# Performance work log

Measured on AMD Instinct MI355X. Metric: run time of the kernel, lower is better.

## Reference

```python
import math
import jax, jax.numpy as jnp
import numpy as np

LMAX = 2


def _cg_complex(j1, m1, j2, m2, j3, m3):
    # Standard (Racah) Clebsch-Gordan coefficient <j1 m1 j2 m2 | j3 m3> for integer l.
    if m1 + m2 != m3 or j3 < abs(j1 - j2) or j3 > j1 + j2:
        return 0.0
    f = math.factorial
    pre = math.sqrt((2 * j3 + 1) * f(j3 + j1 - j2) * f(j3 - j1 + j2) * f(j1 + j2 - j3) / f(j1 + j2 + j3 + 1))
    pre *= math.sqrt(f(j3 + m3) * f(j3 - m3) * f(j1 - m1) * f(j1 + m1) * f(j2 - m2) * f(j2 + m2))
    kmin = max(0, j2 - j3 - m1, j1 + m2 - j3)
    kmax = min(j1 + j2 - j3, j1 - m1, j2 + m2)
    s = 0.0
    for k in range(kmin, kmax + 1):
        s += (-1.0) ** k / (f(k) * f(j1 + j2 - j3 - k) * f(j1 - m1 - k) * f(j2 + m2 - k) * f(j3 - j2 + m1 + k) * f(j3 - j1 - m2 + k))
    return pre * s


def _u_matrix(l):
    # Unitary map from complex SH (Condon-Shortley) to real SH, rows = real mu, cols = complex m.
    U = np.zeros((2 * l + 1, 2 * l + 1), dtype=np.complex128)
    U[l, l] = 1.0
    isq2 = 1.0 / math.sqrt(2.0)
    for m in range(1, l + 1):
        U[l + m, l - m] = isq2
        U[l + m, l + m] = ((-1.0) ** m) * isq2
        U[l - m, l - m] = 1j * isq2
        U[l - m, l + m] = -1j * ((-1.0) ** m) * isq2
    return U


def _real_clebsch_gordan(lmax):
    # Dense real-SH CG tensor over combined s=(l,m) indices, shape [S,S,S], S=(lmax+1)^2.
    S = (lmax + 1) ** 2
    cg = np.zeros((S, S, S))
    for l1 in range(lmax + 1):
        for l2 in range(lmax + 1):
            for l3 in range(abs(l1 - l2), min(lmax, l1 + l2) + 1):
                blk = np.zeros((2 * l1 + 1, 2 * l2 + 1, 2 * l3 + 1))
                for i1, m1 in enumerate(range(-l1, l1 + 1)):
                    for i2, m2 in enumerate(range(-l2, l2 + 1)):
                        for i3, m3 in enumerate(range(-l3, l3 + 1)):
                            blk[i1, i2, i3] = _cg_complex(l1, m1, l2, m2, l3, m3)
                U1, U2, U3 = _u_matrix(l1), _u_matrix(l2), _u_matrix(l3)
                r = np.einsum('am,bn,co,mno->abc', U1, U2, U3.conj(), blk.astype(np.complex128))
                r = r.real if (l1 + l2 + l3) % 2 == 0 else r.imag  # parity-dependent real part
                cg[l1 * l1:(l1 + 1) ** 2, l2 * l2:(l2 + 1) ** 2, l3 * l3:(l3 + 1) ** 2] = r
    return cg


def _sparse_cg(lmax):
    cg = _real_clebsch_gordan(lmax)
    i1, i2, i3 = np.nonzero(np.abs(cg) > 1e-10)
    vals = cg[i1, i2, i3].astype(np.float32)
    widx = np.floor(np.sqrt(i3.astype(np.float64))).astype(np.int32)  # l of output combined index
    return vals, i1.astype(np.int32), i2.astype(np.int32), i3.astype(np.int32), widx


def _spherical_harmonics_l2(d):
    # Real SH up to l=2, 'component' normalization (|x|=1 assumed). Order: (l,m) = (0,0),(1,-1),(1,0),(1,1),(2,-2..2).
    x, y, z = d[..., 0], d[..., 1], d[..., 2]
    s3, s5, s15 = math.sqrt(3.0), math.sqrt(5.0), math.sqrt(15.0)
    return jnp.stack([
        jnp.ones_like(x),
        s3 * y, s3 * z, s3 * x,
        s15 * x * y, s15 * y * z, 0.5 * s5 * (3.0 * z * z - 1.0), s15 * x * z, 0.5 * s15 * (x * x - y * y),
    ], axis=-1)


def setup_inputs():
    N_ATOMS, N_EDGES, N_BASIS, N_RADIAL = 1200, 12000, 128, 20
    S = (LMAX + 1) ** 2
    key = jax.random.key(0)
    ks = jax.random.split(key, 8)
    vals, i1, i2, i3, widx = _sparse_cg(LMAX)
    return {
        'x': jax.random.normal(ks[0], (N_ATOMS, S, N_BASIS), jnp.float32),
        'radial_ij': jax.random.uniform(ks[1], (N_EDGES, N_RADIAL), jnp.float32),
        'dir_ij': jax.random.normal(ks[2], (N_EDGES, 3), jnp.float32),
        'cutoff_ij': jax.random.uniform(ks[3], (N_EDGES, 1), jnp.float32),
        'W_filter': jax.random.normal(ks[6], (N_RADIAL, N_BASIS * (LMAX + 1)), jnp.float32) / math.sqrt(N_RADIAL),
        'b_filter': jnp.zeros((N_BASIS * (LMAX + 1),), jnp.float32),
        'cg_vals': jnp.asarray(vals),
        'idx_i': jax.random.randint(ks[4], (N_EDGES,), 0, N_ATOMS),
        'idx_j': jax.random.randint(ks[5], (N_EDGES,), 0, N_ATOMS),
        'cg_idx_in1': jnp.asarray(i1),
        'cg_idx_in2': jnp.asarray(i2),
        'cg_idx_out': jnp.asarray(i3),
        'w_idx': jnp.asarray(widx),
    }


def reference(x, radial_ij, dir_ij, cutoff_ij, W_filter, b_filter, cg_vals,
              idx_i, idx_j, cg_idx_in1, cg_idx_in2, cg_idx_out, w_idx):
    n_atoms, S, F = x.shape
    E = dir_ij.shape[0]
    d = dir_ij / jnp.linalg.norm(dir_ij, axis=-1, keepdims=True)
    Y = _spherical_harmonics_l2(d)                        # [E, S]
    Wij = (radial_ij @ W_filter + b_filter) * cutoff_ij   # [E, (lmax+1)*F]
    Wij = Wij.reshape(E, LMAX + 1, F)                     # per-l radial filter
    xj = x[idx_j]                                         # [E, S, F] neighbor features
    # Sparse CG tensor-product contraction over combined (l,m) indices.
    v = (Y[:, cg_idx_in2, None] * cg_vals[None, :, None]
         * Wij[:, w_idx, :] * xj[:, cg_idx_in1, :])       # [E, n_cg, F]
    yij = jnp.zeros((E, S, F), v.dtype).at[:, cg_idx_out, :].add(v)
    return jax.ops.segment_sum(yij, idx_i, num_segments=n_atoms)
```

## Files before the change

### kernel.cpp

```cpp
#include <hip/hip_runtime.h>
#include <math.h>


#define S9    9
#define NF    128
#define NRAD  20
#define CHUNK 16

__global__ void hist_kernel(const int* __restrict__ idx_i, int E, int* __restrict__ counts) {
    int e = blockIdx.x * blockDim.x + threadIdx.x;
    if (e < E) atomicAdd(&counts[idx_i[e]], 1);
}

__global__ __launch_bounds__(256) void scan_kernel(const int* __restrict__ counts, int A,
                                                   int* __restrict__ offsets, int* __restrict__ cursor) {
    __shared__ int part[256];
    const int t = threadIdx.x;
    const int base = t * 8;
    int c[8];
    int s = 0;
    #pragma unroll
    for (int p = 0; p < 8; ++p) {
        int idx = base + p;
        c[p] = (idx < A) ? counts[idx] : 0;
        s += c[p];
    }
    part[t] = s;
    __syncthreads();
    #pragma unroll
    for (int off = 1; off < 256; off <<= 1) {
        int v = (t >= off) ? part[t - off] : 0;
        __syncthreads();
        part[t] += v;
        __syncthreads();
    }
    int run = part[t] - s;
    #pragma unroll
    for (int p = 0; p < 8; ++p) {
        int idx = base + p;
        if (idx < A) { offsets[idx] = run; cursor[idx] = run; run += c[p]; }
    }
    if (t == 255) offsets[A] = run;
}

__global__ void scatter_kernel(const int* __restrict__ idx_i, int E,
                               int* __restrict__ cursor, int* __restrict__ esorted) {
    int e = blockIdx.x * blockDim.x + threadIdx.x;
    if (e < E) {
        int p = atomicAdd(&cursor[idx_i[e]], 1);
        esorted[p] = e;
    }
}

__global__ __launch_bounds__(128) void so3_atom_kernel(
    const float* __restrict__ x,
    const float* __restrict__ radial,
    const float* __restrict__ dir,
    const float* __restrict__ cutoff,
    const float* __restrict__ Wf,
    const float* __restrict__ bf,
    const float* __restrict__ cg_vals,
    const int* __restrict__ idx_j,
    const int* __restrict__ cg_i1,
    const int* __restrict__ cg_i2,
    const int* __restrict__ cg_i3,
    int ncg,
    const int* __restrict__ offsets,
    const int* __restrict__ esorted,
    float* __restrict__ out)
{
    const int a = blockIdx.x;
    const int f = threadIdx.x;
    const int start = offsets[a];
    const int end   = offsets[a + 1];

    __shared__ float M[CHUNK][81];
    __shared__ float Ysh[CHUNK][9];
    __shared__ int   els[CHUNK];

    float acc[S9];
    #pragma unroll
    for (int s = 0; s < S9; ++s) acc[s] = 0.0f;

    const float b0 = bf[0 * NF + f];
    const float b1 = bf[1 * NF + f];
    const float b2 = bf[2 * NF + f];

    for (int cs = start; cs < end; cs += CHUNK) {
        const int n = min(CHUNK, end - cs);

        for (int q = f; q < n * 81; q += NF) ((float*)M)[q] = 0.0f;

        if (f < n) {
            const int e = esorted[cs + f];
            els[f] = e;
            float dx = dir[3 * e], dy = dir[3 * e + 1], dz = dir[3 * e + 2];
            const float inv = rsqrtf(dx * dx + dy * dy + dz * dz);
            dx *= inv; dy *= inv; dz *= inv;
            const float s3c  = 1.7320508075688772f;
            const float s5c  = 2.2360679774997896f;
            const float s15c = 3.8729833462074170f;
            Ysh[f][0] = 1.0f;
            Ysh[f][1] = s3c * dy;
            Ysh[f][2] = s3c * dz;
            Ysh[f][3] = s3c * dx;
            Ysh[f][4] = s15c * dx * dy;
            Ysh[f][5] = s15c * dy * dz;
            Ysh[f][6] = 0.5f * s5c * (3.0f * dz * dz - 1.0f);
            Ysh[f][7] = s15c * dx * dz;
            Ysh[f][8] = 0.5f * s15c * (dx * dx - dy * dy);
        }
        __syncthreads();

        for (int c = 0; c < n; ++c) {
            for (int k = f; k < ncg; k += NF) {
                atomicAdd(&M[c][cg_i3[k] * S9 + cg_i1[k]], cg_vals[k] * Ysh[c][cg_i2[k]]);
            }
        }
        __syncthreads();

        for (int c = 0; c < n; ++c) {
            const int e = els[c];

            float rad[NRAD];
            #pragma unroll
            for (int r = 0; r < NRAD; ++r) rad[r] = radial[e * NRAD + r];
            const float cut = cutoff[e];

            float wl0 = b0, wl1 = b1, wl2 = b2;
            #pragma unroll
            for (int r = 0; r < NRAD; ++r) {
                const float* wrow = Wf + r * (3 * NF) + f;
                wl0 = fmaf(rad[r], wrow[0],      wl0);
                wl1 = fmaf(rad[r], wrow[NF],     wl1);
                wl2 = fmaf(rad[r], wrow[2 * NF], wl2);
            }
            wl0 *= cut; wl1 *= cut; wl2 *= cut;

            const int j = idx_j[e];
            const float* xp = x + (size_t)j * (S9 * NF) + f;
            float xj[S9];
            #pragma unroll
            for (int s = 0; s < S9; ++s) xj[s] = xp[s * NF];

            const float* Mc = M[c];
            #pragma unroll
            for (int s3 = 0; s3 < S9; ++s3) {
                float t = 0.0f;
                #pragma unroll
                for (int s1 = 0; s1 < S9; ++s1) t = fmaf(Mc[s3 * S9 + s1], xj[s1], t);
                const float w = (s3 == 0) ? wl0 : ((s3 < 4) ? wl1 : wl2);
                acc[s3] = fmaf(w, t, acc[s3]);
            }
        }
        __syncthreads();
    }

    float* op = out + (size_t)a * (S9 * NF) + f;
    #pragma unroll
    for (int s = 0; s < S9; ++s) op[s * NF] = acc[s];
}

extern "C" void kernel_launch(void* const* d_in, const int* in_sizes, int n_in,
                              void* d_out, int out_size, void* d_ws, size_t ws_size,
                              hipStream_t stream) {
    const float* x       = (const float*)d_in[0];
    const float* radial  = (const float*)d_in[1];
    const float* dir     = (const float*)d_in[2];
    const float* cutoff  = (const float*)d_in[3];
    const float* Wf      = (const float*)d_in[4];
    const float* bf      = (const float*)d_in[5];
    const float* cg_vals = (const float*)d_in[6];
    const int*   idx_i   = (const int*)d_in[7];
    const int*   idx_j   = (const int*)d_in[8];
    const int*   cg_i1   = (const int*)d_in[9];
    const int*   cg_i2   = (const int*)d_in[10];
    const int*   cg_i3   = (const int*)d_in[11];

    const int E   = in_sizes[7];
    const int ncg = in_sizes[6];
    const int A   = in_sizes[0] / (S9 * NF);

    int* counts  = (int*)d_ws;
    int* offsets = counts + A;
    int* cursor  = offsets + (A + 1);
    int* esorted = cursor + A;

    hipMemsetAsync(counts, 0, (size_t)A * sizeof(int), stream);

    const int TB = 256;
    hist_kernel<<<(E + TB - 1) / TB, TB, 0, stream>>>(idx_i, E, counts);
    scan_kernel<<<1, 256, 0, stream>>>(counts, A, offsets, cursor);
    scatter_kernel<<<(E + TB - 1) / TB, TB, 0, stream>>>(idx_i, E, cursor, esorted);

    so3_atom_kernel<<<A, NF, 0, stream>>>(
        x, radial, dir, cutoff, Wf, bf, cg_vals,
        idx_j, cg_i1, cg_i2, cg_i3, ncg, offsets, esorted, (float*)d_out);
}
```

Measured before the change: 144.7 us.

## Split per-atom work into fixed edge chunks with slot reduction pass

Replaces the one-block-per-atom kernel with one 64-thread block per 8-edge chunk. Chunks are found by a second prefix scan over per-atom chunk counts and a binary search in each block. Partial sums are written to workspace slots and summed by a separate reduce kernel, falling back to atomics into a zeroed output when the workspace is too small. It also vectorises features as float2, pads the CG matrix rows for float4 shared-memory loads, and spreads the CG atomic build over 8 lanes per edge. The goal is better load balance and occupancy when atoms have uneven neighbour counts, at the cost of an extra launch and slot traffic.

```diff
diff --git a/kernel.cpp b/kernel.cpp
--- a/kernel.cpp
+++ b/kernel.cpp
@@ -2,10 +2,15 @@
 #include <math.h>
 
 
-#define S9    9
-#define NF    128
-#define NRAD  20
-#define CHUNK 16
+#define S9     9
+#define MROW   12
+#define NF     128
+#define NRAD   20
+#define CEDGE  8
+
+__device__ inline float2 f2fma(float a, float2 b, float2 c) {
+    return make_float2(fmaf(a, b.x, c.x), fmaf(a, b.y, c.y));
+}
 
 __global__ void hist_kernel(const int* __restrict__ idx_i, int E, int* __restrict__ counts) {
     int e = blockIdx.x * blockDim.x + threadIdx.x;
@@ -13,7 +18,8 @@
 }
 
 __global__ __launch_bounds__(256) void scan_kernel(const int* __restrict__ counts, int A,
-                                                   int* __restrict__ offsets, int* __restrict__ cursor) {
+                                                   int* __restrict__ offsets, int* __restrict__ cursor,
+                                                   int* __restrict__ chunk_off) {
     __shared__ int part[256];
     const int t = threadIdx.x;
     const int base = t * 8;
@@ -41,6 +47,32 @@
         if (idx < A) { offsets[idx] = run; cursor[idx] = run; run += c[p]; }
     }
     if (t == 255) offsets[A] = run;
+    __syncthreads();
+
+    int k[8];
+    int s2 = 0;
+    #pragma unroll
+    for (int p = 0; p < 8; ++p) {
+        int idx = base + p;
+        k[p] = (idx < A) ? ((c[p] + CEDGE - 1) / CEDGE) : 0;
+        s2 += k[p];
+    }
+    part[t] = s2;
+    __syncthreads();
+    #pragma unroll
+    for (int off = 1; off < 256; off <<= 1) {
+        int v = (t >= off) ? part[t - off] : 0;
+        __syncthreads();
+        part[t] += v;
+        __syncthreads();
+    }
+    int run2 = part[t] - s2;
+    #pragma unroll
+    for (int p = 0; p < 8; ++p) {
+        int idx = base + p;
+        if (idx < A) { chunk_off[idx] = run2; run2 += k[p]; }
+    }
+    if (t == 255) chunk_off[A] = run2;
 }
 
 __global__ void scatter_kernel(const int* __restrict__ idx_i, int E,
@@ -52,7 +84,7 @@
     }
 }
 
-__global__ __launch_bounds__(128) void so3_atom_kernel(
+__global__ __launch_bounds__(64) void so3_chunk_kernel(
     const float* __restrict__ x,
     const float* __restrict__ radial,
     const float* __restrict__ dir,
@@ -64,101 +96,163 @@
     const int* __restrict__ cg_i1,
     const int* __restrict__ cg_i2,
     const int* __restrict__ cg_i3,
-    int ncg,
+    int ncg, int A,
     const int* __restrict__ offsets,
+    const int* __restrict__ chunk_off,
     const int* __restrict__ esorted,
+    float* __restrict__ slots,
+    float* __restrict__ out,
+    int use_slots)
+{
+    const int ch = blockIdx.x;
+    const int nchunks = chunk_off[A];
+    if (ch >= nchunks) return;
+
+    int lo = 0, hi = A;
+    while (hi - lo > 1) {
+        int mid = (lo + hi) >> 1;
+        if (chunk_off[mid] <= ch) lo = mid; else hi = mid;
+    }
+    const int a = lo;
+    const int q = ch - chunk_off[a];
+    const int estart = offsets[a] + q * CEDGE;
+    const int n = min(CEDGE, offsets[a + 1] - estart);
+
+    const int t = threadIdx.x;
+
+    __shared__ __align__(16) float M[CEDGE][MROW * S9];
+    __shared__ float Ysh[CEDGE][S9];
+    __shared__ int   els[CEDGE];
+
+    {
+        float4* Mz = (float4*)&M[0][0];
+        const int tot4 = CEDGE * MROW * S9 / 4;
+        for (int qq = t; qq < tot4; qq += 64) Mz[qq] = make_float4(0.f, 0.f, 0.f, 0.f);
+    }
+    if (t < n) {
+        const int e = esorted[estart + t];
+        els[t] = e;
+        float dx = dir[3 * e], dy = dir[3 * e + 1], dz = dir[3 * e + 2];
+        const float inv = rsqrtf(dx * dx + dy * dy + dz * dz);
+        dx *= inv; dy *= inv; dz *= inv;
+        const float s3c  = 1.7320508075688772f;
+        const float s5c  = 2.2360679774997896f;
+        const float s15c = 3.8729833462074170f;
+        Ysh[t][0] = 1.0f;
+        Ysh[t][1] = s3c * dy;
+        Ysh[t][2] = s3c * dz;
+        Ysh[t][3] = s3c * dx;
+        Ysh[t][4] = s15c * dx * dy;
+        Ysh[t][5] = s15c * dy * dz;
+        Ysh[t][6] = 0.5f * s5c * (3.0f * dz * dz - 1.0f);
+        Ysh[t][7] = s15c * dx * dz;
+        Ysh[t][8] = 0.5f * s15c * (dx * dx - dy * dy);
+    }
+    __syncthreads();
+
+    {
+        const int c = t >> 3;
+        const int r = t & 7;
+        if (c < n) {
+            for (int kk = r; kk < ncg; kk += 8) {
+                atomicAdd(&M[c][cg_i3[kk] * MROW + cg_i1[kk]], cg_vals[kk] * Ysh[c][cg_i2[kk]]);
+            }
+        }
+    }
+    __syncthreads();
+
+    float2 acc[S9];
+    #pragma unroll
+    for (int s = 0; s < S9; ++s) acc[s] = make_float2(0.f, 0.f);
+
+    const float2 b0 = ((const float2*)(bf + 0 * NF))[t];
+    const float2 b1 = ((const float2*)(bf + 1 * NF))[t];
+    const float2 b2 = ((const float2*)(bf + 2 * NF))[t];
+
+    for (int c = 0; c < n; ++c) {
+        int e = __builtin_amdgcn_readfirstlane(els[c]);
+        const int j = __builtin_amdgcn_readfirstlane(idx_j[e]);
+        const float cut = cutoff[e];
+
+        float rad[NRAD];
+        #pragma unroll
+        for (int r = 0; r < NRAD; ++r) rad[r] = radial[e * NRAD + r];
+
+        float2 wl0 = b0, wl1 = b1, wl2 = b2;
+        #pragma unroll
+        for (int r = 0; r < NRAD; ++r) {
+            const float2* wrow = (const float2*)(Wf + r * (3 * NF));
+            wl0 = f2fma(rad[r], wrow[t],            wl0);
+            wl1 = f2fma(rad[r], wrow[t + 64],       wl1);
+            wl2 = f2fma(rad[r], wrow[t + 128],      wl2);
+        }
+        wl0.x *= cut; wl0.y *= cut; wl1.x *= cut; wl1.y *= cut; wl2.x *= cut; wl2.y *= cut;
+
+        const float2* xp = (const float2*)(x + (size_t)j * (S9 * NF)) + t;
+        float2 xj[S9];
+        #pragma unroll
+        for (int s = 0; s < S9; ++s) xj[s] = xp[s * 64];
+
+        #pragma unroll
+        for (int s3 = 0; s3 < S9; ++s3) {
+            const float4* mr = (const float4*)&M[c][s3 * MROW];
+            const float4 m0 = mr[0];
+            const float4 m1 = mr[1];
+            const float  m8 = M[c][s3 * MROW + 8];
+            float2 tsum = make_float2(0.f, 0.f);
+            tsum = f2fma(m0.x, xj[0], tsum);
+            tsum = f2fma(m0.y, xj[1], tsum);
+            tsum = f2fma(m0.z, xj[2], tsum);
+            tsum = f2fma(m0.w, xj[3], tsum);
+            tsum = f2fma(m1.x, xj[4], tsum);
+            tsum = f2fma(m1.y, xj[5], tsum);
+            tsum = f2fma(m1.z, xj[6], tsum);
+            tsum = f2fma(m1.w, xj[7], tsum);
+            tsum = f2fma(m8,   xj[8], tsum);
+            const float2 w = (s3 == 0) ? wl0 : ((s3 < 4) ? wl1 : wl2);
+            acc[s3].x = fmaf(w.x, tsum.x, acc[s3].x);
+            acc[s3].y = fmaf(w.y, tsum.y, acc[s3].y);
+        }
+    }
+
+    if (use_slots) {
+        float2* sp = (float2*)(slots + (size_t)ch * (S9 * NF)) + t;
+        #pragma unroll
+        for (int s = 0; s < S9; ++s) sp[s * 64] = acc[s];
+    } else {
+        float* op = out + (size_t)a * (S9 * NF) + 2 * t;
+        #pragma unroll
+        for (int s = 0; s < S9; ++s) {
+            atomicAdd(&op[s * NF],     acc[s].x);
+            atomicAdd(&op[s * NF + 1], acc[s].y);
+        }
+    }
+}
+
+__global__ __launch_bounds__(64) void so3_reduce_kernel(
+    const float* __restrict__ slots, const int* __restrict__ chunk_off,
     float* __restrict__ out)
 {
     const int a = blockIdx.x;
-    const int f = threadIdx.x;
-    const int start = offsets[a];
-    const int end   = offsets[a + 1];
-
-    __shared__ float M[CHUNK][81];
-    __shared__ float Ysh[CHUNK][9];
-    __shared__ int   els[CHUNK];
-
-    float acc[S9];
-    #pragma unroll
-    for (int s = 0; s < S9; ++s) acc[s] = 0.0f;
-
-    const float b0 = bf[0 * NF + f];
-    const float b1 = bf[1 * NF + f];
-    const float b2 = bf[2 * NF + f];
-
-    for (int cs = start; cs < end; cs += CHUNK) {
-        const int n = min(CHUNK, end - cs);
-
-        for (int q = f; q < n * 81; q += NF) ((float*)M)[q] = 0.0f;
-
-        if (f < n) {
-            const int e = esorted[cs + f];
-            els[f] = e;
-            float dx = dir[3 * e], dy = dir[3 * e + 1], dz = dir[3 * e + 2];
-            const float inv = rsqrtf(dx * dx + dy * dy + dz * dz);
-            dx *= inv; dy *= inv; dz *= inv;
-            const float s3c  = 1.7320508075688772f;
-            const float s5c  = 2.2360679774997896f;
-            const float s15c = 3.8729833462074170f;
-            Ysh[f][0] = 1.0f;
-            Ysh[f][1] = s3c * dy;
-            Ysh[f][2] = s3c * dz;
-            Ysh[f][3] = s3c * dx;
-            Ysh[f][4] = s15c * dx * dy;
-            Ysh[f][5] = s15c * dy * dz;
-            Ysh[f][6] = 0.5f * s5c * (3.0f * dz * dz - 1.0f);
-            Ysh[f][7] = s15c * dx * dz;
-            Ysh[f][8] = 0.5f * s15c * (dx * dx - dy * dy);
-        }
-        __syncthreads();
-
-        for (int c = 0; c < n; ++c) {
-            for (int k = f; k < ncg; k += NF) {
-                atomicAdd(&M[c][cg_i3[k] * S9 + cg_i1[k]], cg_vals[k] * Ysh[c][cg_i2[k]]);
-            }
-        }
-        __syncthreads();
-
-        for (int c = 0; c < n; ++c) {
-            const int e = els[c];
-
-            float rad[NRAD];
-            #pragma unroll
-            for (int r = 0; r < NRAD; ++r) rad[r] = radial[e * NRAD + r];
-            const float cut = cutoff[e];
-
-            float wl0 = b0, wl1 = b1, wl2 = b2;
-            #pragma unroll
-            for (int r = 0; r < NRAD; ++r) {
-                const float* wrow = Wf + r * (3 * NF) + f;
-                wl0 = fmaf(rad[r], wrow[0],      wl0);
-                wl1 = fmaf(rad[r], wrow[NF],     wl1);
-                wl2 = fmaf(rad[r], wrow[2 * NF], wl2);
-            }
-            wl0 *= cut; wl1 *= cut; wl2 *= cut;
-
-            const int j = idx_j[e];
-            const float* xp = x + (size_t)j * (S9 * NF) + f;
-            float xj[S9];
-            #pragma unroll
-            for (int s = 0; s < S9; ++s) xj[s] = xp[s * NF];
-
-            const float* Mc = M[c];
-            #pragma unroll
-            for (int s3 = 0; s3 < S9; ++s3) {
-                float t = 0.0f;
-                #pragma unroll
-                for (int s1 = 0; s1 < S9; ++s1) t = fmaf(Mc[s3 * S9 + s1], xj[s1], t);
-                const float w = (s3 == 0) ? wl0 : ((s3 < 4) ? wl1 : wl2);
-                acc[s3] = fmaf(w, t, acc[s3]);
-            }
-        }
-        __syncthreads();
-    }
-
-    float* op = out + (size_t)a * (S9 * NF) + f;
-    #pragma unroll
-    for (int s = 0; s < S9; ++s) op[s * NF] = acc[s];
+    const int t = threadIdx.x;
+    const int c0 = chunk_off[a];
+    const int c1 = chunk_off[a + 1];
+
+    float2 acc[S9];
+    #pragma unroll
+    for (int s = 0; s < S9; ++s) acc[s] = make_float2(0.f, 0.f);
+
+    for (int ch = c0; ch < c1; ++ch) {
+        const float2* sp = (const float2*)(slots + (size_t)ch * (S9 * NF)) + t;
+        #pragma unroll
+        for (int s = 0; s < S9; ++s) {
+            float2 v = sp[s * 64];
+            acc[s].x += v.x; acc[s].y += v.y;
+        }
+    }
+    float2* op = (float2*)(out + (size_t)a * (S9 * NF)) + t;
+    #pragma unroll
+    for (int s = 0; s < S9; ++s) op[s * 64] = acc[s];
 }
 
 extern "C" void kernel_launch(void* const* d_in, const int* in_sizes, int n_in,
@@ -181,19 +275,37 @@
     const int ncg = in_sizes[6];
     const int A   = in_sizes[0] / (S9 * NF);
 
-    int* counts  = (int*)d_ws;
-    int* offsets = counts + A;
-    int* cursor  = offsets + (A + 1);
-    int* esorted = cursor + A;
+    int* counts    = (int*)d_ws;
+    int* offsets   = counts + A;
+    int* cursor    = offsets + (A + 1);
+    int* chunk_off = cursor + A;
+    int* esorted   = chunk_off + (A + 1);
+    size_t int_bytes = (size_t)(4 * A + 2 + E) * sizeof(int);
+    size_t slots_off = (int_bytes + 255) & ~(size_t)255;
+
+    const int max_chunks = E / CEDGE + A;
+    size_t slots_bytes = (size_t)max_chunks * (S9 * NF) * sizeof(float);
+    const int use_slots = (ws_size >= slots_off + slots_bytes) ? 1 : 0;
+    float* slots = (float*)((char*)d_ws + slots_off);
+    float* out   = (float*)d_out;
 
     hipMemsetAsync(counts, 0, (size_t)A * sizeof(int), stream);
 
     const int TB = 256;
     hist_kernel<<<(E + TB - 1) / TB, TB, 0, stream>>>(idx_i, E, counts);
-    scan_kernel<<<1, 256, 0, stream>>>(counts, A, offsets, cursor);
+    scan_kernel<<<1, 256, 0, stream>>>(counts, A, offsets, cursor, chunk_off);
     scatter_kernel<<<(E + TB - 1) / TB, TB, 0, stream>>>(idx_i, E, cursor, esorted);
 
-    so3_atom_kernel<<<A, NF, 0, stream>>>(
-        x, radial, dir, cutoff, Wf, bf, cg_vals,
-        idx_j, cg_i1, cg_i2, cg_i3, ncg, offsets, esorted, (float*)d_out);
-}
+    if (!use_slots) {
+        hipMemsetAsync(out, 0, (size_t)out_size * sizeof(float), stream);
+    }
+
+    so3_chunk_kernel<<<max_chunks, 64, 0, stream>>>(
+        x, radial, dir, cutoff, Wf, bf, cg_vals, idx_j,
+        cg_i1, cg_i2, cg_i3, ncg, A, offsets, chunk_off, esorted,
+        slots, out, use_slots);
+
+    if (use_slots) {
+        so3_reduce_kernel<<<A, 64, 0, stream>>>(slots, chunk_off, out);
+    }
+}
```

Result: faster. 126.4 us (-12.6%).
